# Kernel tuning notes

Hardware: AMD Instinct MI355X
Metric: run time of the kernel (lower is better)

Reference implementation:

```python
import jax, jax.numpy as jnp
import numpy as np

NNODE = 500000       # nodes -> 2*NNODE global DOFs
NELEM = 500000       # elements, 8 DOF each (2D quad)
NDOF = 2 * NNODE


def setup_inputs() -> dict:
    key = jax.random.key(0)
    k1, k2, k3, k4 = jax.random.split(key, 4)
    u = jax.random.normal(k1, (NDOF,), dtype=jnp.float32)
    weight1 = jax.random.normal(k2, (NDOF,), dtype=jnp.float32)
    bc_idx = jnp.arange(NDOF, dtype=jnp.int64)  # free-DOF indices (all free)
    # elemental DOF map: 8 global DOF indices per element (irregular)
    edof = jax.random.randint(k3, (NELEM, 8), 0, NDOF, dtype=jnp.int64)
    # per-element 8x8 stiffness matrices
    stiffness = jax.random.normal(k4, (NELEM, 8, 8), dtype=jnp.float32)
    return {"u": u, "weight1": weight1, "bc_idx": bc_idx,
            "edof": edof, "stiffness": stiffness}


def reference(u, weight1, bc_idx, edof, stiffness):
    # u1 = zeros; u1[bc_idx] = weight1 * u[bc_idx]
    u1 = jnp.zeros_like(u).at[bc_idx].set(weight1 * u[bc_idx])
    # gather elemental DOF values: [E, 8]
    ue = u1[edof]
    # per-element stiffness matvec: [E, 8]
    fe = jnp.einsum('eij,ej->ei', stiffness, ue)
    # scatter-add assembly into global force vector
    F = jnp.zeros_like(u).at[edof.reshape(-1)].add(fe.reshape(-1))
    return F
```

## Files before the change

### kernel.cpp

```cpp
#include <hip/hip_runtime.h>

typedef float          vfloat4  __attribute__((ext_vector_type(4)));
typedef int            vint4    __attribute__((ext_vector_type(4)));
typedef unsigned short vushort4 __attribute__((ext_vector_type(4)));

#define BSHIFT 12
#define BSIZE  4096
#define G1     512
#define TPBC   1024
#define TPB    256

__global__ void scatter_u1_kernel(const float* __restrict__ u,
                                  const float* __restrict__ w1,
                                  const int* __restrict__ bc,
                                  float* __restrict__ u1, int n) {
    int k = blockIdx.x * blockDim.x + threadIdx.x;
    if (k < n) {
        int idx = bc[k];
        u1[idx] = w1[k] * u[idx];
    }
}

__global__ void compute_fe_hist_kernel(const float* __restrict__ u1,
                                       const int* __restrict__ edof,
                                       const float* __restrict__ stiff,
                                       unsigned short* __restrict__ febuf16,
                                       int* __restrict__ cnt,
                                       int total, int nb, int chunk) {
    __shared__ int h[256];
    int wg = blockIdx.x;
    if (threadIdx.x < nb) h[threadIdx.x] = 0;
    __syncthreads();
    int k0 = wg * chunk;
    int k1 = min(k0 + chunk, total);
    for (int k = k0 + threadIdx.x; k < k1; k += TPBC) {
        int e = k >> 3;
        int i = k & 7;
        int idx = __builtin_nontemporal_load(edof + k);
        float ue = u1[idx];

        const vfloat4* Kr = (const vfloat4*)(stiff + (size_t)e * 64 + (size_t)i * 8);
        vfloat4 ka = __builtin_nontemporal_load(Kr);
        vfloat4 kb = __builtin_nontemporal_load(Kr + 1);

        float fe;
        fe  = ka.x * __shfl(ue, 0, 8);
        fe += ka.y * __shfl(ue, 1, 8);
        fe += ka.z * __shfl(ue, 2, 8);
        fe += ka.w * __shfl(ue, 3, 8);
        fe += kb.x * __shfl(ue, 4, 8);
        fe += kb.y * __shfl(ue, 5, 8);
        fe += kb.z * __shfl(ue, 6, 8);
        fe += kb.w * __shfl(ue, 7, 8);

        unsigned short hu = __builtin_bit_cast(unsigned short, (_Float16)fe);
        __builtin_nontemporal_store(hu, febuf16 + k);
        atomicAdd(&h[idx >> BSHIFT], 1);
    }
    __syncthreads();
    if (threadIdx.x < nb) cnt[threadIdx.x * G1 + wg] = h[threadIdx.x];
}

__global__ void scan_bucket_kernel(const int* __restrict__ cnt,
                                   int* __restrict__ wgoff,
                                   int* __restrict__ btot) {
    int b = blockIdx.x;
    int lane = threadIdx.x;
    const int per = G1 / 64;
    int v[per];
    int s = 0;
    for (int j = 0; j < per; ++j) { v[j] = cnt[b * G1 + lane * per + j]; s += v[j]; }
    int incl = s;
    for (int off = 1; off < 64; off <<= 1) {
        int n = __shfl_up(incl, off, 64);
        if (lane >= off) incl += n;
    }
    int run = incl - s;
    for (int j = 0; j < per; ++j) { wgoff[b * G1 + lane * per + j] = run; run += v[j]; }
    if (lane == 63) btot[b] = incl;
}

__global__ void scan_total_kernel(const int* __restrict__ btot,
                                  int* __restrict__ bstart, int nb) {
    int lane = threadIdx.x;
    int v[4];
    int s = 0;
    for (int j = 0; j < 4; ++j) {
        int i = lane * 4 + j;
        v[j] = (i < nb) ? btot[i] : 0;
        s += v[j];
    }
    int incl = s;
    for (int off = 1; off < 64; off <<= 1) {
        int n = __shfl_up(incl, off, 64);
        if (lane >= off) incl += n;
    }
    int run = incl - s;
    for (int j = 0; j < 4; ++j) {
        int i = lane * 4 + j;
        if (i < nb) bstart[i] = run;
        run += v[j];
    }
    if (lane == 63) bstart[nb] = incl;
}

__global__ void scatter_pairs_kernel(const int* __restrict__ edof,
                                     const unsigned short* __restrict__ febuf16,
                                     const int* __restrict__ wgoff,
                                     const int* __restrict__ bstart,
                                     unsigned int* __restrict__ pairs,
                                     int total, int nb, int chunk) {
    __shared__ int base[256];
    int wg = blockIdx.x;
    if (threadIdx.x < nb)
        base[threadIdx.x] = bstart[threadIdx.x] + wgoff[threadIdx.x * G1 + wg];
    __syncthreads();
    int k0 = wg * chunk;
    int k1 = min(k0 + chunk, total);
    for (int k = k0 + threadIdx.x * 4; k < k1; k += TPBC * 4) {
        vint4    idx = __builtin_nontemporal_load((const vint4*)(edof + k));
        vushort4 hv  = __builtin_nontemporal_load((const vushort4*)(febuf16 + k));
        int      ids[4] = {idx.x, idx.y, idx.z, idx.w};
        unsigned hus[4] = {hv.x, hv.y, hv.z, hv.w};
        #pragma unroll
        for (int j = 0; j < 4; ++j) {
            int id = ids[j];
            int b = id >> BSHIFT;
            int pos = atomicAdd(&base[b], 1);
            pairs[pos] = ((unsigned)(id & (BSIZE - 1)) << 16) | hus[j];
        }
    }
}

__global__ void bucket_reduce_kernel(const unsigned int* __restrict__ pairs,
                                     const int* __restrict__ bstart,
                                     float* __restrict__ F, int ndof) {
    __shared__ float acc[BSIZE];
    int b = blockIdx.x;
    for (int j = threadIdx.x; j < BSIZE; j += 512) acc[j] = 0.0f;
    __syncthreads();
    int k0 = bstart[b], k1 = bstart[b + 1];
    for (int k = k0 + threadIdx.x; k < k1; k += 512) {
        unsigned p = pairs[k];
        float fe = (float)__builtin_bit_cast(_Float16, (unsigned short)(p & 0xffffu));
        atomicAdd(&acc[p >> 16], fe);
    }
    __syncthreads();
    int gbase = b << BSHIFT;
    for (int j = threadIdx.x; j < BSIZE; j += 512) {
        int g = gbase + j;
        if (g < ndof) F[g] = acc[j];
    }
}

__global__ void elem_assemble_kernel(const float* __restrict__ u1,
                                     const int* __restrict__ edof,
                                     const float* __restrict__ stiff,
                                     float* __restrict__ F, int nelem) {
    int t = blockIdx.x * blockDim.x + threadIdx.x;
    int e = t >> 3;
    if (e >= nelem) return;
    int i = t & 7;
    int idx = __builtin_nontemporal_load(edof + t);
    float ue = u1[idx];
    const vfloat4* Kr = (const vfloat4*)(stiff + (size_t)e * 64 + (size_t)i * 8);
    vfloat4 k0 = __builtin_nontemporal_load(Kr);
    vfloat4 k1 = __builtin_nontemporal_load(Kr + 1);
    float fe;
    fe  = k0.x * __shfl(ue, 0, 8);
    fe += k0.y * __shfl(ue, 1, 8);
    fe += k0.z * __shfl(ue, 2, 8);
    fe += k0.w * __shfl(ue, 3, 8);
    fe += k1.x * __shfl(ue, 4, 8);
    fe += k1.y * __shfl(ue, 5, 8);
    fe += k1.z * __shfl(ue, 6, 8);
    fe += k1.w * __shfl(ue, 7, 8);
    unsafeAtomicAdd(&F[idx], fe);
}

extern "C" void kernel_launch(void* const* d_in, const int* in_sizes, int n_in,
                              void* d_out, int out_size, void* d_ws, size_t ws_size,
                              hipStream_t stream) {
    const float* u     = (const float*)d_in[0];
    const float* w1    = (const float*)d_in[1];
    const int*   bc    = (const int*)d_in[2];
    const int*   edof  = (const int*)d_in[3];
    const float* stiff = (const float*)d_in[4];
    float* F = (float*)d_out;

    int ndof  = in_sizes[0];
    int nbc   = in_sizes[2];
    int total = in_sizes[3];
    int nelem = total / 8;
    int nb    = (ndof + BSIZE - 1) >> BSHIFT;

    char* w = (char*)d_ws;
    size_t o = 0;
    auto take = [&](size_t nbytes) -> char* {
        char* p = w + o;
        o += (nbytes + 255) & ~(size_t)255;
        return p;
    };
    float* u1 = (float*)take((size_t)ndof * 4);
    unsigned short* febuf16 = (unsigned short*)take((size_t)total * 2);
    unsigned int* pairs = (unsigned int*)take((size_t)total * 4);
    int* cnt    = (int*)take((size_t)nb * G1 * 4);
    int* wgoff  = (int*)take((size_t)nb * G1 * 4);
    int* btot   = (int*)take((size_t)nb * 4);
    int* bstart = (int*)take((size_t)(nb + 1) * 4);

    (void)hipMemsetAsync(u1, 0, (size_t)ndof * sizeof(float), stream);
    scatter_u1_kernel<<<(nbc + TPB - 1) / TPB, TPB, 0, stream>>>(u, w1, bc, u1, nbc);

    if (o <= ws_size && nb <= 256 && total % 8 == 0) {
        int chunk = (((total + G1 - 1) / G1) + TPBC * 4 - 1) & ~(TPBC * 4 - 1);
        compute_fe_hist_kernel<<<G1, TPBC, 0, stream>>>(
            u1, edof, stiff, febuf16, cnt, total, nb, chunk);
        scan_bucket_kernel<<<nb, 64, 0, stream>>>(cnt, wgoff, btot);
        scan_total_kernel<<<1, 64, 0, stream>>>(btot, bstart, nb);
        scatter_pairs_kernel<<<G1, TPBC, 0, stream>>>(
            edof, febuf16, wgoff, bstart, pairs, total, nb, chunk);
        bucket_reduce_kernel<<<nb, 512, 0, stream>>>(pairs, bstart, F, ndof);
    } else {
        (void)hipMemsetAsync(F, 0, (size_t)ndof * sizeof(float), stream);
        elem_assemble_kernel<<<(total + TPB - 1) / TPB, TPB, 0, stream>>>(
            u1, edof, stiff, F, nelem);
    }
}
```

Before: 289.3 us.

## Move element matvec into scatter pass and make histogram pass index-only

The histogram pass now reads only edof, using vectorized int4 loads. The per-element stiffness matvec moves into the scatter pass, which packs pairs directly, so the fp16 intermediate buffer is no longer written and re-read. The bucket reduce also rises from 512 to 1024 threads per block. The histogram loop requires k+4<=k1 and would drop a tail if a chunk were not a multiple of 4, though chunk sizes here are multiples of 4096.

```diff
diff --git a/kernel.cpp b/kernel.cpp
--- a/kernel.cpp
+++ b/kernel.cpp
@@ -2,7 +2,6 @@
 
 typedef float          vfloat4  __attribute__((ext_vector_type(4)));
 typedef int            vint4    __attribute__((ext_vector_type(4)));
-typedef unsigned short vushort4 __attribute__((ext_vector_type(4)));
 
 #define BSHIFT 12
 #define BSIZE  4096
@@ -21,41 +20,21 @@
     }
 }
 
-__global__ void compute_fe_hist_kernel(const float* __restrict__ u1,
-                                       const int* __restrict__ edof,
-                                       const float* __restrict__ stiff,
-                                       unsigned short* __restrict__ febuf16,
-                                       int* __restrict__ cnt,
-                                       int total, int nb, int chunk) {
+__global__ void hist_kernel(const int* __restrict__ edof,
+                            int* __restrict__ cnt,
+                            int total, int nb, int chunk) {
     __shared__ int h[256];
     int wg = blockIdx.x;
     if (threadIdx.x < nb) h[threadIdx.x] = 0;
     __syncthreads();
     int k0 = wg * chunk;
     int k1 = min(k0 + chunk, total);
-    for (int k = k0 + threadIdx.x; k < k1; k += TPBC) {
-        int e = k >> 3;
-        int i = k & 7;
-        int idx = __builtin_nontemporal_load(edof + k);
-        float ue = u1[idx];
-
-        const vfloat4* Kr = (const vfloat4*)(stiff + (size_t)e * 64 + (size_t)i * 8);
-        vfloat4 ka = __builtin_nontemporal_load(Kr);
-        vfloat4 kb = __builtin_nontemporal_load(Kr + 1);
-
-        float fe;
-        fe  = ka.x * __shfl(ue, 0, 8);
-        fe += ka.y * __shfl(ue, 1, 8);
-        fe += ka.z * __shfl(ue, 2, 8);
-        fe += ka.w * __shfl(ue, 3, 8);
-        fe += kb.x * __shfl(ue, 4, 8);
-        fe += kb.y * __shfl(ue, 5, 8);
-        fe += kb.z * __shfl(ue, 6, 8);
-        fe += kb.w * __shfl(ue, 7, 8);
-
-        unsigned short hu = __builtin_bit_cast(unsigned short, (_Float16)fe);
-        __builtin_nontemporal_store(hu, febuf16 + k);
-        atomicAdd(&h[idx >> BSHIFT], 1);
+    for (int k = k0 + threadIdx.x * 4; k + 4 <= k1; k += TPBC * 4) {
+        vint4 idx = __builtin_nontemporal_load((const vint4*)(edof + k));
+        atomicAdd(&h[idx.x >> BSHIFT], 1);
+        atomicAdd(&h[idx.y >> BSHIFT], 1);
+        atomicAdd(&h[idx.z >> BSHIFT], 1);
+        atomicAdd(&h[idx.w >> BSHIFT], 1);
     }
     __syncthreads();
     if (threadIdx.x < nb) cnt[threadIdx.x * G1 + wg] = h[threadIdx.x];
@@ -104,12 +83,13 @@
     if (lane == 63) bstart[nb] = incl;
 }
 
-__global__ void scatter_pairs_kernel(const int* __restrict__ edof,
-                                     const unsigned short* __restrict__ febuf16,
-                                     const int* __restrict__ wgoff,
-                                     const int* __restrict__ bstart,
-                                     unsigned int* __restrict__ pairs,
-                                     int total, int nb, int chunk) {
+__global__ void compute_scatter_kernel(const float* __restrict__ u1,
+                                       const int* __restrict__ edof,
+                                       const float* __restrict__ stiff,
+                                       const int* __restrict__ wgoff,
+                                       const int* __restrict__ bstart,
+                                       unsigned int* __restrict__ pairs,
+                                       int total, int nb, int chunk) {
     __shared__ int base[256];
     int wg = blockIdx.x;
     if (threadIdx.x < nb)
@@ -117,18 +97,30 @@
     __syncthreads();
     int k0 = wg * chunk;
     int k1 = min(k0 + chunk, total);
-    for (int k = k0 + threadIdx.x * 4; k < k1; k += TPBC * 4) {
-        vint4    idx = __builtin_nontemporal_load((const vint4*)(edof + k));
-        vushort4 hv  = __builtin_nontemporal_load((const vushort4*)(febuf16 + k));
-        int      ids[4] = {idx.x, idx.y, idx.z, idx.w};
-        unsigned hus[4] = {hv.x, hv.y, hv.z, hv.w};
-        #pragma unroll
-        for (int j = 0; j < 4; ++j) {
-            int id = ids[j];
-            int b = id >> BSHIFT;
-            int pos = atomicAdd(&base[b], 1);
-            pairs[pos] = ((unsigned)(id & (BSIZE - 1)) << 16) | hus[j];
-        }
+    for (int k = k0 + threadIdx.x; k < k1; k += TPBC) {
+        int e = k >> 3;
+        int i = k & 7;
+        int idx = __builtin_nontemporal_load(edof + k);
+        float ue = u1[idx];
+
+        const vfloat4* Kr = (const vfloat4*)(stiff + (size_t)e * 64 + (size_t)i * 8);
+        vfloat4 ka = __builtin_nontemporal_load(Kr);
+        vfloat4 kb = __builtin_nontemporal_load(Kr + 1);
+
+        float fe;
+        fe  = ka.x * __shfl(ue, 0, 8);
+        fe += ka.y * __shfl(ue, 1, 8);
+        fe += ka.z * __shfl(ue, 2, 8);
+        fe += ka.w * __shfl(ue, 3, 8);
+        fe += kb.x * __shfl(ue, 4, 8);
+        fe += kb.y * __shfl(ue, 5, 8);
+        fe += kb.z * __shfl(ue, 6, 8);
+        fe += kb.w * __shfl(ue, 7, 8);
+
+        unsigned short hu = __builtin_bit_cast(unsigned short, (_Float16)fe);
+        int b = idx >> BSHIFT;
+        int pos = atomicAdd(&base[b], 1);
+        pairs[pos] = ((unsigned)(idx & (BSIZE - 1)) << 16) | (unsigned)hu;
     }
 }
 
@@ -137,17 +129,17 @@
                                      float* __restrict__ F, int ndof) {
     __shared__ float acc[BSIZE];
     int b = blockIdx.x;
-    for (int j = threadIdx.x; j < BSIZE; j += 512) acc[j] = 0.0f;
+    for (int j = threadIdx.x; j < BSIZE; j += 1024) acc[j] = 0.0f;
     __syncthreads();
     int k0 = bstart[b], k1 = bstart[b + 1];
-    for (int k = k0 + threadIdx.x; k < k1; k += 512) {
+    for (int k = k0 + threadIdx.x; k < k1; k += 1024) {
         unsigned p = pairs[k];
         float fe = (float)__builtin_bit_cast(_Float16, (unsigned short)(p & 0xffffu));
         atomicAdd(&acc[p >> 16], fe);
     }
     __syncthreads();
     int gbase = b << BSHIFT;
-    for (int j = threadIdx.x; j < BSIZE; j += 512) {
+    for (int j = threadIdx.x; j < BSIZE; j += 1024) {
         int g = gbase + j;
         if (g < ndof) F[g] = acc[j];
     }
@@ -202,7 +194,6 @@
         return p;
     };
     float* u1 = (float*)take((size_t)ndof * 4);
-    unsigned short* febuf16 = (unsigned short*)take((size_t)total * 2);
     unsigned int* pairs = (unsigned int*)take((size_t)total * 4);
     int* cnt    = (int*)take((size_t)nb * G1 * 4);
     int* wgoff  = (int*)take((size_t)nb * G1 * 4);
@@ -214,13 +205,12 @@
 
     if (o <= ws_size && nb <= 256 && total % 8 == 0) {
         int chunk = (((total + G1 - 1) / G1) + TPBC * 4 - 1) & ~(TPBC * 4 - 1);
-        compute_fe_hist_kernel<<<G1, TPBC, 0, stream>>>(
-            u1, edof, stiff, febuf16, cnt, total, nb, chunk);
+        hist_kernel<<<G1, TPBC, 0, stream>>>(edof, cnt, total, nb, chunk);
         scan_bucket_kernel<<<nb, 64, 0, stream>>>(cnt, wgoff, btot);
         scan_total_kernel<<<1, 64, 0, stream>>>(btot, bstart, nb);
-        scatter_pairs_kernel<<<G1, TPBC, 0, stream>>>(
-            edof, febuf16, wgoff, bstart, pairs, total, nb, chunk);
-        bucket_reduce_kernel<<<nb, 512, 0, stream>>>(pairs, bstart, F, ndof);
+        compute_scatter_kernel<<<G1, TPBC, 0, stream>>>(
+            u1, edof, stiff, wgoff, bstart, pairs, total, nb, chunk);
+        bucket_reduce_kernel<<<nb, 1024, 0, stream>>>(pairs, bstart, F, ndof);
     } else {
         (void)hipMemsetAsync(F, 0, (size_t)ndof * sizeof(float), stream);
         elem_assemble_kernel<<<(total + TPB - 1) / TPB, TPB, 0, stream>>>(
```

New measurement: 311.8 us. +7.8%, slower.
